# Kernel tuning notes

Measured on AMD Instinct MI355X. Metric: run time of the kernel, lower is better.

## Reference

```python
import jax, jax.numpy as jnp
import numpy as np

EMBED = 768
HEADS = 12
HEAD_DIM = EMBED // HEADS  # 64


def setup_inputs() -> dict:
    key = jax.random.key(0)
    ks = jax.random.split(key, 9)
    d = HEAD_DIM
    s = 1.0 / np.sqrt(d)
    return {
        "x": jax.random.normal(ks[0], (8, 1024, EMBED), dtype=jnp.float32),
        "ln_w": jnp.ones((EMBED,), dtype=jnp.float32),
        "ln_b": jnp.zeros((EMBED,), dtype=jnp.float32),
        "Wq": jax.random.uniform(ks[1], (d, d), jnp.float32, -s, s),
        "bq": jax.random.uniform(ks[2], (d,), jnp.float32, -s, s),
        "Wk": jax.random.uniform(ks[3], (d, d), jnp.float32, -s, s),
        "bk": jax.random.uniform(ks[4], (d,), jnp.float32, -s, s),
        "Wv": jax.random.uniform(ks[5], (d, d), jnp.float32, -s, s),
        "bv": jax.random.uniform(ks[6], (d,), jnp.float32, -s, s),
    }


def reference(x, ln_w, ln_b, Wq, bq, Wk, bk, Wv, bv):
    bs, n, e = x.shape
    # LayerNorm over last dim (eps matches torch default 1e-5)
    mu = jnp.mean(x, axis=-1, keepdims=True)
    var = jnp.mean(jnp.square(x - mu), axis=-1, keepdims=True)
    xn = (x - mu) / jnp.sqrt(var + 1e-5) * ln_w + ln_b
    # Raw view split (NOT transpose split): [bs, n, E] -> [bs, H, n, d]
    xh = xn.reshape(bs, HEADS, n, HEAD_DIM)
    # Linear layers (torch Linear: y = x @ W.T + b)
    q = jnp.einsum("bhnd,ed->bhne", xh, Wq) + bq
    k = jnp.einsum("bhnd,ed->bhne", xh, Wk) + bk
    v = jnp.einsum("bhnd,ed->bhne", xh, Wv) + bv
    # Unusual: softmax FIRST, then divide by sqrt(d)
    scores = jnp.einsum("bhqd,bhkd->bhqk", q, k)
    attn = jax.nn.softmax(scores, axis=-1) / jnp.sqrt(jnp.float32(HEAD_DIM))
    feature = jnp.einsum("bhqk,bhkd->bhqd", attn, v)
    return feature.reshape(bs, n, e)
```

## Files before the change

kernel.cpp:

```cpp
#include <hip/hip_runtime.h>

#define EMBED 768
#define HEADS 12
#define HD 64
#define SEQ 1024
#define BS 8
#define NROWS (BS * HEADS * SEQ)
#define XP 72
#define PLP 40

typedef _Float16 f16;
typedef f16 f16x4 __attribute__((ext_vector_type(4)));
typedef f16 f16x8 __attribute__((ext_vector_type(8)));
typedef float f32x4 __attribute__((ext_vector_type(4)));

__global__ __launch_bounds__(256) void k_lnstats(const float* __restrict__ x,
                                                 float* __restrict__ mu_out,
                                                 float* __restrict__ rs_out) {
    const int w = threadIdx.x >> 6;
    const int lane = threadIdx.x & 63;
    const int row = blockIdx.x * 4 + w;
    const float4* xr = (const float4*)(x + (long)row * EMBED);
    float s = 0.f, sq = 0.f;
#pragma unroll
    for (int kk = 0; kk < 3; ++kk) {
        float4 v = xr[lane + kk * 64];
        s += v.x + v.y + v.z + v.w;
        sq += v.x * v.x + v.y * v.y + v.z * v.z + v.w * v.w;
    }
#pragma unroll
    for (int off = 32; off; off >>= 1) {
        s += __shfl_xor(s, off, 64);
        sq += __shfl_xor(sq, off, 64);
    }
    if (lane == 0) {
        float mu = s * (1.f / EMBED);
        float var = sq * (1.f / EMBED) - mu * mu;
        mu_out[row] = mu;
        rs_out[row] = rsqrtf(var + 1e-5f);
    }
}

__global__ __launch_bounds__(256) void k_qkv(
    const float* __restrict__ x, const float* __restrict__ lw, const float* __restrict__ lb,
    const float* __restrict__ Wq, const float* __restrict__ bq,
    const float* __restrict__ Wk, const float* __restrict__ bk,
    const float* __restrict__ Wv, const float* __restrict__ bv,
    const float* __restrict__ mu, const float* __restrict__ rs,
    f16* __restrict__ qo, f16* __restrict__ ko, f16* __restrict__ vo) {
    __shared__ __align__(16) f16 xh[64 * XP];
    __shared__ __align__(16) f16 wl[3][64 * XP];
    const int t = threadIdx.x;
    const unsigned r0 = (unsigned)blockIdx.x * 64;
    const int bh = (int)(r0 >> 10);
    const int seq0 = (int)(r0 & 1023);

    const float* Ws[3] = {Wq, Wk, Wv};
#pragma unroll
    for (int m = 0; m < 3; ++m) {
        const int base = t * 16;
        const int row = base >> 6, col = base & 63;
        const float4* src = (const float4*)(Ws[m] + base);
        f16* dst = &wl[m][row * XP + col];
#pragma unroll
        for (int j = 0; j < 4; ++j) {
            float4 vv = src[j];
            f16x4 h = {(f16)vv.x, (f16)vv.y, (f16)vv.z, (f16)vv.w};
            *(f16x4*)(dst + j * 4) = h;
        }
    }
    {
        const unsigned fb = r0 * 64u + (unsigned)t * 16u;
        const unsigned xrow = fb / EMBED;
        const unsigned c0 = fb % EMBED;
        const float m_ = mu[xrow], s_ = rs[xrow];
        const int lrow = (t * 16) >> 6, lcol = (t * 16) & 63;
        f16* dst = &xh[lrow * XP + lcol];
        const float4* xp = (const float4*)(x + fb);
        const float4* wp = (const float4*)(lw + c0);
        const float4* bp = (const float4*)(lb + c0);
#pragma unroll
        for (int j = 0; j < 4; ++j) {
            float4 xv = xp[j], wv = wp[j], bv2 = bp[j];
            f16x4 h = {(f16)((xv.x - m_) * s_ * wv.x + bv2.x), (f16)((xv.y - m_) * s_ * wv.y + bv2.y),
                       (f16)((xv.z - m_) * s_ * wv.z + bv2.z), (f16)((xv.w - m_) * s_ * wv.w + bv2.w)};
            *(f16x4*)(dst + j * 4) = h;
        }
    }
    __syncthreads();

    const int lane = t & 63, w = t >> 6, l16 = lane & 15, quad = lane >> 4;
    f16x8 a0 = *(const f16x8*)&xh[(w * 16 + l16) * XP + quad * 8];
    f16x8 a1 = *(const f16x8*)&xh[(w * 16 + l16) * XP + 32 + quad * 8];
    const float* Bs[3] = {bq, bk, bv};
    f32x4 acc[3][4];
#pragma unroll
    for (int m = 0; m < 3; ++m) {
#pragma unroll
        for (int nt = 0; nt < 4; ++nt) {
            f16x8 b0 = *(const f16x8*)&wl[m][(nt * 16 + l16) * XP + quad * 8];
            f16x8 b1 = *(const f16x8*)&wl[m][(nt * 16 + l16) * XP + 32 + quad * 8];
            f32x4 a = {0.f, 0.f, 0.f, 0.f};
            a = __builtin_amdgcn_mfma_f32_16x16x32_f16(a0, b0, a, 0, 0, 0);
            a = __builtin_amdgcn_mfma_f32_16x16x32_f16(a1, b1, a, 0, 0, 0);
            const float bias = Bs[m][nt * 16 + l16];
#pragma unroll
            for (int rg = 0; rg < 4; ++rg) a[rg] += bias;
            acc[m][nt] = a;
        }
    }

#pragma unroll
    for (int m = 0; m < 3; ++m) {
        __syncthreads();
        if (m < 2) {
#pragma unroll
            for (int nt = 0; nt < 4; ++nt)
#pragma unroll
                for (int rg = 0; rg < 4; ++rg)
                    xh[(w * 16 + quad * 4 + rg) * XP + nt * 16 + l16] = (f16)acc[m][nt][rg];
        } else {
#pragma unroll
            for (int nt = 0; nt < 4; ++nt) {
                f16x4 h = {(f16)acc[m][nt][0], (f16)acc[m][nt][1], (f16)acc[m][nt][2], (f16)acc[m][nt][3]};
                *(f16x4*)&xh[(nt * 16 + l16) * XP + w * 16 + quad * 4] = h;
            }
        }
        __syncthreads();
        if (m == 0) {
#pragma unroll
            for (int c = t; c < 512; c += 256) {
                const int row = c >> 3, c8 = (c & 7) * 8;
                *(f16x8*)(qo + ((long)r0 + row) * 64 + c8) = *(const f16x8*)&xh[row * XP + c8];
            }
        } else if (m == 1) {
#pragma unroll
            for (int c = t; c < 512; c += 256) {
                const int row = c >> 3, c8 = (c & 7) * 8;
                const int seq = seq0 + row;
                const int tile = seq >> 5;
                const int l16s = seq & 15, r16 = (seq >> 4) & 1;
                const int cseg = c8 >> 5, qd = (c8 >> 3) & 3;
                const long dst = ((long)bh << 16) + tile * 2048 + (r16 * 2 + cseg) * 512 + qd * 128 + l16s * 8;
                *(f16x8*)(ko + dst) = *(const f16x8*)&xh[row * XP + c8];
            }
        } else {
#pragma unroll
            for (int c = t; c < 512; c += 256) {
                const int d = c >> 3, s8 = (c & 7) * 8;
                const int seq = seq0 + s8;
                const int tile = seq >> 5;
                const int qd = (seq & 31) >> 3;
                const int nt = d >> 4, l16d = d & 15;
                const long dst = ((long)bh << 16) + tile * 2048 + nt * 512 + qd * 128 + l16d * 8;
                *(f16x8*)(vo + dst) = *(const f16x8*)&xh[d * XP + s8];
            }
        }
    }
}

__global__ __launch_bounds__(256) void k_attn(const f16* __restrict__ q,
                                              const f16* __restrict__ k,
                                              const f16* __restrict__ vt,
                                              float* __restrict__ out) {
    __shared__ __align__(16) f16 pl[4][32 * PLP];
    const int t = threadIdx.x;
    const int w = t >> 6, lane = t & 63, l16 = lane & 15, quad = lane >> 4;
    const int bh = blockIdx.x;
    const int q0 = blockIdx.y * 128 + w * 32;
    const long hb = (long)bh * SEQ;
    const f16* kp0 = k + ((long)bh << 16) + lane * 8;
    const f16* vp0 = vt + ((long)bh << 16) + lane * 8;

    f16x8 qf[2][2];
#pragma unroll
    for (int mt = 0; mt < 2; ++mt) {
        const f16* qp = q + (hb + q0 + mt * 16 + l16) * 64 + quad * 8;
        qf[mt][0] = *(const f16x8*)qp;
        qf[mt][1] = *(const f16x8*)(qp + 32);
    }
    f32x4 o[2][4];
    f32x4 ls[2];
#pragma unroll
    for (int mt = 0; mt < 2; ++mt) {
        ls[mt] = (f32x4){0.f, 0.f, 0.f, 0.f};
#pragma unroll
        for (int nt = 0; nt < 4; ++nt) o[mt][nt] = (f32x4){0.f, 0.f, 0.f, 0.f};
    }
    f16x8 one;
#pragma unroll
    for (int j = 0; j < 8; ++j) one[j] = (f16)1.0f;

#define LOADK(kt, kf)                                  \
    {                                                  \
        const f16* kp = kp0 + (kt) * 2048;             \
        kf[0] = *(const f16x8*)kp;                     \
        kf[1] = *(const f16x8*)(kp + 512);             \
        kf[2] = *(const f16x8*)(kp + 1024);            \
        kf[3] = *(const f16x8*)(kp + 1536);            \
    }
#define LOADV(kt, vf)                                  \
    {                                                  \
        const f16* vp = vp0 + (kt) * 2048;             \
        vf[0] = *(const f16x8*)vp;                     \
        vf[1] = *(const f16x8*)(vp + 512);             \
        vf[2] = *(const f16x8*)(vp + 1024);            \
        vf[3] = *(const f16x8*)(vp + 1536);            \
    }

    f16x8 ka[4], va[4], kb[4], vb[4];
    LOADK(0, ka);
    LOADV(0, va);

    auto body = [&](const f16x8* kf, const f16x8* vf) {
        f32x4 s[2][2];
#pragma unroll
        for (int mt = 0; mt < 2; ++mt) {
            f32x4 a = {0.f, 0.f, 0.f, 0.f};
            a = __builtin_amdgcn_mfma_f32_16x16x32_f16(qf[mt][0], kf[0], a, 0, 0, 0);
            a = __builtin_amdgcn_mfma_f32_16x16x32_f16(qf[mt][1], kf[1], a, 0, 0, 0);
            s[mt][0] = a;
            f32x4 b = {0.f, 0.f, 0.f, 0.f};
            b = __builtin_amdgcn_mfma_f32_16x16x32_f16(qf[mt][0], kf[2], b, 0, 0, 0);
            b = __builtin_amdgcn_mfma_f32_16x16x32_f16(qf[mt][1], kf[3], b, 0, 0, 0);
            s[mt][1] = b;
        }
#pragma unroll
        for (int mt = 0; mt < 2; ++mt)
#pragma unroll
            for (int ct = 0; ct < 2; ++ct)
#pragma unroll
                for (int rg = 0; rg < 4; ++rg) {
                    float p = __expf(s[mt][ct][rg] - 14.f);
                    pl[w][(mt * 16 + quad * 4 + rg) * PLP + ct * 16 + l16] = (f16)p;
                }
        f16x8 pf0 = *(const f16x8*)&pl[w][l16 * PLP + quad * 8];
        f16x8 pf1 = *(const f16x8*)&pl[w][(16 + l16) * PLP + quad * 8];
        ls[0] = __builtin_amdgcn_mfma_f32_16x16x32_f16(pf0, one, ls[0], 0, 0, 0);
        ls[1] = __builtin_amdgcn_mfma_f32_16x16x32_f16(pf1, one, ls[1], 0, 0, 0);
#pragma unroll
        for (int nt = 0; nt < 4; ++nt) {
            o[0][nt] = __builtin_amdgcn_mfma_f32_16x16x32_f16(pf0, vf[nt], o[0][nt], 0, 0, 0);
            o[1][nt] = __builtin_amdgcn_mfma_f32_16x16x32_f16(pf1, vf[nt], o[1][nt], 0, 0, 0);
        }
    };

    for (int kt = 0; kt < SEQ / 32; kt += 2) {
        LOADK(kt + 1, kb);
        LOADV(kt + 1, vb);
        body(ka, va);
        const int kn = (kt + 2 < SEQ / 32) ? kt + 2 : SEQ / 32 - 1;
        LOADK(kn, ka);
        LOADV(kn, va);
        body(kb, vb);
    }
#undef LOADK
#undef LOADV

#pragma unroll
    for (int mt = 0; mt < 2; ++mt) {
        float inv[4];
#pragma unroll
        for (int rg = 0; rg < 4; ++rg) inv[rg] = 1.f / (ls[mt][rg] * 8.0f);
#pragma unroll
        for (int nt = 0; nt < 4; ++nt) {
            float* op = out + (hb + q0 + mt * 16 + quad * 4) * 64 + nt * 16 + l16;
#pragma unroll
            for (int rg = 0; rg < 4; ++rg) op[(long)rg * 64] = o[mt][nt][rg] * inv[rg];
        }
    }
}

extern "C" void kernel_launch(void* const* d_in, const int* in_sizes, int n_in,
                              void* d_out, int out_size, void* d_ws, size_t ws_size,
                              hipStream_t stream) {
    const float* x = (const float*)d_in[0];
    const float* lw = (const float*)d_in[1];
    const float* lb = (const float*)d_in[2];
    const float* Wq = (const float*)d_in[3];
    const float* bq = (const float*)d_in[4];
    const float* Wk = (const float*)d_in[5];
    const float* bk = (const float*)d_in[6];
    const float* Wv = (const float*)d_in[7];
    const float* bv = (const float*)d_in[8];
    float* out = (float*)d_out;

    char* ws = (char*)d_ws;
    float* mu = (float*)ws;
    float* rs = (float*)(ws + 32768);
    f16* qo = (f16*)(ws + 65536);
    f16* ko = qo + (long)NROWS * 64;
    f16* vo = ko + (long)NROWS * 64;

    k_lnstats<<<2048, 256, 0, stream>>>(x, mu, rs);
    k_qkv<<<NROWS / 64, 256, 0, stream>>>(x, lw, lb, Wq, bq, Wk, bk, Wv, bv, mu, rs, qo, ko, vo);
    k_attn<<<dim3(BS * HEADS, SEQ / 128), 256, 0, stream>>>(qo, ko, vo, out);
}
```

Measured before the change: 146.1 us.

## Stage K/V tiles cooperatively into double-buffered LDS via global_load_lds

The attention kernel now has the block's four waves cooperatively copy each 32-key K and V tile straight from global memory into a double-buffered shared-memory area using global_load_lds. Each wave then reads its K/V fragments from LDS. Before, every wave fetched the same tiles from global memory through its own registers. The aim is to cut redundant global/L2 traffic by four and free the registers used for prefetching. In exchange, every tile now needs a block-wide barrier plus extra LDS reads, and correctness depends on the barrier waiting for the asynchronous LDS loads to complete.

```diff
diff --git a/kernel.cpp b/kernel.cpp
--- a/kernel.cpp
+++ b/kernel.cpp
@@ -13,6 +13,9 @@
 typedef f16 f16x4 __attribute__((ext_vector_type(4)));
 typedef f16 f16x8 __attribute__((ext_vector_type(8)));
 typedef float f32x4 __attribute__((ext_vector_type(4)));
+
+typedef const __attribute__((address_space(1))) unsigned int gu32;
+typedef __attribute__((address_space(3))) unsigned int lu32;
 
 __global__ __launch_bounds__(256) void k_lnstats(const float* __restrict__ x,
                                                  float* __restrict__ mu_out,
@@ -163,14 +166,27 @@
                                               const f16* __restrict__ k,
                                               const f16* __restrict__ vt,
                                               float* __restrict__ out) {
+    __shared__ __align__(16) f16 kv[2][2][2048];
     __shared__ __align__(16) f16 pl[4][32 * PLP];
     const int t = threadIdx.x;
     const int w = t >> 6, lane = t & 63, l16 = lane & 15, quad = lane >> 4;
     const int bh = blockIdx.x;
     const int q0 = blockIdx.y * 128 + w * 32;
     const long hb = (long)bh * SEQ;
-    const f16* kp0 = k + ((long)bh << 16) + lane * 8;
-    const f16* vp0 = vt + ((long)bh << 16) + lane * 8;
+    const f16* kg = k + ((long)bh << 16);
+    const f16* vg = vt + ((long)bh << 16);
+
+    auto stage = [&](int kt, int buf) {
+#pragma unroll
+        for (int j = 0; j < 2; ++j) {
+            const int c = w * 2 + j;
+            const f16* src = ((c < 4) ? kg : vg) + (long)kt * 2048 + (c & 3) * 512 + lane * 8;
+            f16* dst = &kv[buf][c >> 2][(c & 3) * 512];
+            __builtin_amdgcn_global_load_lds((gu32*)(const void*)src, (lu32*)(void*)dst, 16, 0, 0);
+        }
+    };
+
+    stage(0, 0);
 
     f16x8 qf[2][2];
 #pragma unroll
@@ -191,28 +207,13 @@
 #pragma unroll
     for (int j = 0; j < 8; ++j) one[j] = (f16)1.0f;
 
-#define LOADK(kt, kf)                                  \
-    {                                                  \
-        const f16* kp = kp0 + (kt) * 2048;             \
-        kf[0] = *(const f16x8*)kp;                     \
-        kf[1] = *(const f16x8*)(kp + 512);             \
-        kf[2] = *(const f16x8*)(kp + 1024);            \
-        kf[3] = *(const f16x8*)(kp + 1536);            \
-    }
-#define LOADV(kt, vf)                                  \
-    {                                                  \
-        const f16* vp = vp0 + (kt) * 2048;             \
-        vf[0] = *(const f16x8*)vp;                     \
-        vf[1] = *(const f16x8*)(vp + 512);             \
-        vf[2] = *(const f16x8*)(vp + 1024);            \
-        vf[3] = *(const f16x8*)(vp + 1536);            \
-    }
-
-    f16x8 ka[4], va[4], kb[4], vb[4];
-    LOADK(0, ka);
-    LOADV(0, va);
-
-    auto body = [&](const f16x8* kf, const f16x8* vf) {
+    auto body = [&](int buf) {
+        f16x8 kf[4], vf[4];
+#pragma unroll
+        for (int c = 0; c < 4; ++c) {
+            kf[c] = *(const f16x8*)&kv[buf][0][c * 512 + lane * 8];
+            vf[c] = *(const f16x8*)&kv[buf][1][c * 512 + lane * 8];
+        }
         f32x4 s[2][2];
 #pragma unroll
         for (int mt = 0; mt < 2; ++mt) {
@@ -245,17 +246,14 @@
         }
     };
 
-    for (int kt = 0; kt < SEQ / 32; kt += 2) {
-        LOADK(kt + 1, kb);
-        LOADV(kt + 1, vb);
-        body(ka, va);
-        const int kn = (kt + 2 < SEQ / 32) ? kt + 2 : SEQ / 32 - 1;
-        LOADK(kn, ka);
-        LOADV(kn, va);
-        body(kb, vb);
-    }
-#undef LOADK
-#undef LOADV
+    __syncthreads();
+    int buf = 0;
+    for (int kt = 0; kt < SEQ / 32; ++kt) {
+        if (kt + 1 < SEQ / 32) stage(kt + 1, buf ^ 1);
+        body(buf);
+        __syncthreads();
+        buf ^= 1;
+    }
 
 #pragma unroll
     for (int mt = 0; mt < 2; ++mt) {
```

New measurement: 153.5 us. 1.05x slower.

## Pre-pack QKV weights to fp16 fragment layout once and set MFMA wave priority

Applied to the files above, without the earlier changes.

The first kernel now also converts Wq/Wk/Wv to fp16 in MFMA fragment order, written to workspace. The QKV kernel then loads B fragments straight from global memory and no longer stages all three weight matrices through LDS in every block, which cuts LDS use and per-block conversion work and may raise occupancy. The attention loop wraps its MFMA sections in s_setprio so waves issuing matrix ops get scheduling priority over waves doing exp work. This adds a dependency between kernels and repeated global or L2 reads of the packed weights.

```diff
diff --git a/kernel.cpp b/kernel.cpp
--- a/kernel.cpp
+++ b/kernel.cpp
@@ -15,8 +15,12 @@
 typedef float f32x4 __attribute__((ext_vector_type(4)));
 
 __global__ __launch_bounds__(256) void k_lnstats(const float* __restrict__ x,
+                                                 const float* __restrict__ Wq,
+                                                 const float* __restrict__ Wk,
+                                                 const float* __restrict__ Wv,
                                                  float* __restrict__ mu_out,
-                                                 float* __restrict__ rs_out) {
+                                                 float* __restrict__ rs_out,
+                                                 f16* __restrict__ wf) {
     const int w = threadIdx.x >> 6;
     const int lane = threadIdx.x & 63;
     const int row = blockIdx.x * 4 + w;
@@ -39,36 +43,36 @@
         mu_out[row] = mu;
         rs_out[row] = rsqrtf(var + 1e-5f);
     }
+    if (blockIdx.x < 3) {
+        const float* W = (blockIdx.x == 0) ? Wq : (blockIdx.x == 1) ? Wk : Wv;
+        f16* dst = wf + (long)blockIdx.x * 4096;
+        const int t = threadIdx.x;
+#pragma unroll
+        for (int i = 0; i < 2; ++i) {
+            const int o = t * 2 + i;
+            const int nt = o >> 7, half = (o >> 6) & 1, lp = o & 63;
+            const int qd = lp >> 4, l16 = lp & 15;
+            const float* src = W + (nt * 16 + l16) * 64 + half * 32 + qd * 8;
+            float4 v0 = *(const float4*)src, v1 = *(const float4*)(src + 4);
+            f16x8 h = {(f16)v0.x, (f16)v0.y, (f16)v0.z, (f16)v0.w,
+                       (f16)v1.x, (f16)v1.y, (f16)v1.z, (f16)v1.w};
+            *(f16x8*)(dst + o * 8) = h;
+        }
+    }
 }
 
 __global__ __launch_bounds__(256) void k_qkv(
     const float* __restrict__ x, const float* __restrict__ lw, const float* __restrict__ lb,
-    const float* __restrict__ Wq, const float* __restrict__ bq,
-    const float* __restrict__ Wk, const float* __restrict__ bk,
-    const float* __restrict__ Wv, const float* __restrict__ bv,
+    const f16* __restrict__ wf,
+    const float* __restrict__ bq, const float* __restrict__ bk, const float* __restrict__ bv,
     const float* __restrict__ mu, const float* __restrict__ rs,
     f16* __restrict__ qo, f16* __restrict__ ko, f16* __restrict__ vo) {
     __shared__ __align__(16) f16 xh[64 * XP];
-    __shared__ __align__(16) f16 wl[3][64 * XP];
     const int t = threadIdx.x;
     const unsigned r0 = (unsigned)blockIdx.x * 64;
     const int bh = (int)(r0 >> 10);
     const int seq0 = (int)(r0 & 1023);
 
-    const float* Ws[3] = {Wq, Wk, Wv};
-#pragma unroll
-    for (int m = 0; m < 3; ++m) {
-        const int base = t * 16;
-        const int row = base >> 6, col = base & 63;
-        const float4* src = (const float4*)(Ws[m] + base);
-        f16* dst = &wl[m][row * XP + col];
-#pragma unroll
-        for (int j = 0; j < 4; ++j) {
-            float4 vv = src[j];
-            f16x4 h = {(f16)vv.x, (f16)vv.y, (f16)vv.z, (f16)vv.w};
-            *(f16x4*)(dst + j * 4) = h;
-        }
-    }
     {
         const unsigned fb = r0 * 64u + (unsigned)t * 16u;
         const unsigned xrow = fb / EMBED;
@@ -93,36 +97,35 @@
     f16x8 a0 = *(const f16x8*)&xh[(w * 16 + l16) * XP + quad * 8];
     f16x8 a1 = *(const f16x8*)&xh[(w * 16 + l16) * XP + 32 + quad * 8];
     const float* Bs[3] = {bq, bk, bv};
-    f32x4 acc[3][4];
+
 #pragma unroll
     for (int m = 0; m < 3; ++m) {
+        const f16* wfm = wf + (long)m * 4096 + lane * 8;
+        f32x4 acc[4];
 #pragma unroll
         for (int nt = 0; nt < 4; ++nt) {
-            f16x8 b0 = *(const f16x8*)&wl[m][(nt * 16 + l16) * XP + quad * 8];
-            f16x8 b1 = *(const f16x8*)&wl[m][(nt * 16 + l16) * XP + 32 + quad * 8];
+            f16x8 b0 = *(const f16x8*)(wfm + (nt * 2 + 0) * 512);
+            f16x8 b1 = *(const f16x8*)(wfm + (nt * 2 + 1) * 512);
             f32x4 a = {0.f, 0.f, 0.f, 0.f};
             a = __builtin_amdgcn_mfma_f32_16x16x32_f16(a0, b0, a, 0, 0, 0);
             a = __builtin_amdgcn_mfma_f32_16x16x32_f16(a1, b1, a, 0, 0, 0);
             const float bias = Bs[m][nt * 16 + l16];
 #pragma unroll
             for (int rg = 0; rg < 4; ++rg) a[rg] += bias;
-            acc[m][nt] = a;
-        }
-    }
-
-#pragma unroll
-    for (int m = 0; m < 3; ++m) {
+            acc[nt] = a;
+        }
+
         __syncthreads();
         if (m < 2) {
 #pragma unroll
             for (int nt = 0; nt < 4; ++nt)
 #pragma unroll
                 for (int rg = 0; rg < 4; ++rg)
-                    xh[(w * 16 + quad * 4 + rg) * XP + nt * 16 + l16] = (f16)acc[m][nt][rg];
+                    xh[(w * 16 + quad * 4 + rg) * XP + nt * 16 + l16] = (f16)acc[nt][rg];
         } else {
 #pragma unroll
             for (int nt = 0; nt < 4; ++nt) {
-                f16x4 h = {(f16)acc[m][nt][0], (f16)acc[m][nt][1], (f16)acc[m][nt][2], (f16)acc[m][nt][3]};
+                f16x4 h = {(f16)acc[nt][0], (f16)acc[nt][1], (f16)acc[nt][2], (f16)acc[nt][3]};
                 *(f16x4*)&xh[(nt * 16 + l16) * XP + w * 16 + quad * 4] = h;
             }
         }
@@ -214,6 +217,7 @@
 
     auto body = [&](const f16x8* kf, const f16x8* vf) {
         f32x4 s[2][2];
+        __builtin_amdgcn_s_setprio(1);
 #pragma unroll
         for (int mt = 0; mt < 2; ++mt) {
             f32x4 a = {0.f, 0.f, 0.f, 0.f};
@@ -225,6 +229,7 @@
             b = __builtin_amdgcn_mfma_f32_16x16x32_f16(qf[mt][1], kf[3], b, 0, 0, 0);
             s[mt][1] = b;
         }
+        __builtin_amdgcn_s_setprio(0);
 #pragma unroll
         for (int mt = 0; mt < 2; ++mt)
 #pragma unroll
@@ -236,6 +241,7 @@
                 }
         f16x8 pf0 = *(const f16x8*)&pl[w][l16 * PLP + quad * 8];
         f16x8 pf1 = *(const f16x8*)&pl[w][(16 + l16) * PLP + quad * 8];
+        __builtin_amdgcn_s_setprio(1);
         ls[0] = __builtin_amdgcn_mfma_f32_16x16x32_f16(pf0, one, ls[0], 0, 0, 0);
         ls[1] = __builtin_amdgcn_mfma_f32_16x16x32_f16(pf1, one, ls[1], 0, 0, 0);
 #pragma unroll
@@ -243,6 +249,7 @@
             o[0][nt] = __builtin_amdgcn_mfma_f32_16x16x32_f16(pf0, vf[nt], o[0][nt], 0, 0, 0);
             o[1][nt] = __builtin_amdgcn_mfma_f32_16x16x32_f16(pf1, vf[nt], o[1][nt], 0, 0, 0);
         }
+        __builtin_amdgcn_s_setprio(0);
     };
 
     for (int kt = 0; kt < SEQ / 32; kt += 2) {
@@ -288,11 +295,12 @@
     char* ws = (char*)d_ws;
     float* mu = (float*)ws;
     float* rs = (float*)(ws + 32768);
-    f16* qo = (f16*)(ws + 65536);
+    f16* wfr = (f16*)(ws + 65536);
+    f16* qo = (f16*)(ws + 98304);
     f16* ko = qo + (long)NROWS * 64;
     f16* vo = ko + (long)NROWS * 64;
 
-    k_lnstats<<<2048, 256, 0, stream>>>(x, mu, rs);
-    k_qkv<<<NROWS / 64, 256, 0, stream>>>(x, lw, lb, Wq, bq, Wk, bk, Wv, bv, mu, rs, qo, ko, vo);
+    k_lnstats<<<2048, 256, 0, stream>>>(x, Wq, Wk, Wv, mu, rs, wfr);
+    k_qkv<<<NROWS / 64, 256, 0, stream>>>(x, lw, lb, wfr, bq, bk, bv, mu, rs, qo, ko, vo);
     k_attn<<<dim3(BS * HEADS, SEQ / 128), 256, 0, stream>>>(qo, ko, vo, out);
 }
```

Result: no change. 144.0 us (-1.5%).
